# Kernel optimization log

Hardware: AMD Instinct MI355X
Metric: run time of the kernel (lower is better)

The kernel has to match this reference:

```python
import jax, jax.numpy as jnp
import numpy as np


def _dwconv3d(x, w, b):
    # depthwise Conv3d, kernel 3, stride 1, padding 1 (SAME), groups = channels
    groups = x.shape[1]
    y = jax.lax.conv_general_dilated(
        x, w, window_strides=(1, 1, 1), padding='SAME',
        feature_group_count=groups,
        dimension_numbers=('NCDHW', 'OIDHW', 'NCDHW'))
    return y + b[None, :, None, None, None]


def setup_inputs() -> dict:
    key = jax.random.key(0)
    ks = jax.random.split(key, 8)
    B, C, K, D, H, W = 4, 64, 64, 16, 64, 64
    sc = 0.1
    return {
        'x_q': jax.random.normal(ks[0], (B, C, D, H, W), jnp.float32),
        'x_kv': jax.random.normal(ks[1], (B, K, D, H, W), jnp.float32),
        'wq': jax.random.normal(ks[2], (C, 1, 3, 3, 3), jnp.float32) * sc,
        'bq': jax.random.normal(ks[3], (C,), jnp.float32) * sc,
        'wk': jax.random.normal(ks[4], (K, 1, 3, 3, 3), jnp.float32) * sc,
        'bk': jax.random.normal(ks[5], (K,), jnp.float32) * sc,
        'wv': jax.random.normal(ks[6], (K, 1, 3, 3, 3), jnp.float32) * sc,
        'bv': jax.random.normal(ks[7], (K,), jnp.float32) * sc,
    }


def reference(x_q, x_kv, wq, bq, wk, bk, wv, bv):
    q = _dwconv3d(x_q, wq, bq)   # [B,C,D,H,W]
    k = _dwconv3d(x_kv, wk, bk)  # [B,K,D,H,W]
    v = _dwconv3d(x_kv, wv, bv)  # [B,K,D,H,W]
    B, C = q.shape[:2]
    K = k.shape[1]
    qf = q.reshape(B, C, -1)     # [B,C,S]
    kf = k.reshape(B, K, -1)     # [B,K,S]
    vf = v.reshape(B, K, -1)     # [B,K,S]
    attn = jnp.einsum('bcs,bks->bck', qf, kf) / jnp.sqrt(jnp.asarray(K, qf.dtype))
    attn = jax.nn.softmax(attn, axis=-1)           # [B,C,K]
    n = int(0.1 * C)
    at = attn.transpose(0, 2, 1)                   # [B,K,C]
    _, idx = jax.lax.top_k(at, n)                  # [B,K,n] indices into C
    mask = jnp.sum(jax.nn.one_hot(idx, C, dtype=attn.dtype), axis=-2)  # [B,K,C]
    attn_m = attn * mask.transpose(0, 2, 1)        # [B,C,K], NOT renormalized
    out = jnp.einsum('bck,bks->bcs', attn_m, vf).reshape(q.shape)
    return x_q + out, attn_m
```

## Files before the change

### kernel.cpp

```cpp
#include <hip/hip_runtime.h>
#include <math.h>

#define BB   4
#define CC   64
#define KK   64
#define DDim 16
#define HDim 64
#define WDim 64
#define SS   (DDim*HDim*WDim)
#define PLANE (HDim*WDim)
#define NCH2 64
#define TOPN 6
#define RSTR 68
#define RROWS 18
#define NSTG 288

typedef __attribute__((ext_vector_type(8))) short bf16x8;
typedef __attribute__((ext_vector_type(4))) float f32x4;

__device__ __forceinline__ unsigned cvt_pk_bf16(float lo, float hi) {
    unsigned r;
    asm("v_cvt_pk_bf16_f32 %0, %1, %2" : "=v"(r) : "v"(lo), "v"(hi));
    return r;
}
__device__ __forceinline__ float bf2f(unsigned short u) {
    union { unsigned u; float f; } v; v.u = ((unsigned)u) << 16; return v.f;
}

__global__ __launch_bounds__(128) void conv_uni(
    const float* __restrict__ xq, const float* __restrict__ xkv,
    const float* __restrict__ wq, const float* __restrict__ bq,
    const float* __restrict__ wk, const float* __restrict__ bk,
    const float* __restrict__ wv, const float* __restrict__ bv,
    unsigned short* __restrict__ qo, unsigned short* __restrict__ ko,
    unsigned short* __restrict__ vo)
{
    __shared__ float ringQ[4][RROWS*RSTR];
    __shared__ float ringK[4][RROWS*RSTR];

    int bid  = blockIdx.x;
    int work = (bid & 7) * 128 + (bid >> 3);
    int b  = work >> 8;
    int c  = (work >> 2) & 63;
    int hq = work & 3;
    int g0 = hq << 4;

    const float* srcQ = xq  + (size_t)(b*CC + c) * SS;
    const float* srcK = xkv + (size_t)(b*CC + c) * SS;
    float wQ[27], wK[27], wV[27];
    #pragma unroll
    for (int i = 0; i < 27; ++i) {
        wQ[i] = wq[c*27 + i];
        wK[i] = wk[c*27 + i];
        wV[i] = wv[c*27 + i];
    }
    const float bQ = bq[c], bK = bk[c], bV = bv[c];

    unsigned short* dQ = qo + (size_t)(b*CC + c) * SS;
    unsigned short* dK = ko + (size_t)(b*CC + c) * SS;
    unsigned short* dV = vo + (size_t)(b*CC + c) * SS;

    const int tid  = threadIdx.x;
    const int lane = tid & 63;
    const int wg   = tid & 7;
    const int w0   = wg << 3;
    const int hl   = tid >> 3;
    const int y    = g0 + hl;

    float4 stgQ[3], stgK[3];
#define SLOAD2(p) {                                                            \
    const int p_ = (p);                                                        \
    const bool pv_ = (p_ >= 0 && p_ < DDim);                                   \
    _Pragma("unroll")                                                          \
    for (int i_ = 0; i_ < 3; ++i_) {                                           \
        const int fidx_ = i_*128 + tid;                                        \
        const int row_  = fidx_ >> 4;                                          \
        const int gy_   = g0 - 1 + row_;                                       \
        float4 vq_ = make_float4(0.f,0.f,0.f,0.f), vk_ = vq_;                  \
        if (pv_ && fidx_ < NSTG && gy_ >= 0 && gy_ < HDim) {                   \
            const size_t o_ = (size_t)p_*PLANE + gy_*WDim + (fidx_ & 15)*4;    \
            vq_ = *(const float4*)(srcQ + o_);                                 \
            vk_ = *(const float4*)(srcK + o_);                                 \
        }                                                                      \
        stgQ[i_] = vq_; stgK[i_] = vk_;                                        \
    } }
#define SWRITE2(p) {                                                           \
    float* RQ_ = ringQ[(p) & 3];                                               \
    float* RK_ = ringK[(p) & 3];                                               \
    _Pragma("unroll")                                                          \
    for (int i_ = 0; i_ < 3; ++i_) {                                           \
        const int fidx_ = i_*128 + tid;                                        \
        if (fidx_ < NSTG) {                                                    \
            const int off_ = (fidx_ >> 4)*RSTR + (fidx_ & 15)*4;               \
            *(float4*)&RQ_[off_] = stgQ[i_];                                   \
            *(float4*)&RK_[off_] = stgK[i_];                                   \
        }                                                                      \
    } }

#define COMPUTE_D(dd) {                                                        \
    float accQ[8], accK[8], accV[8];                                           \
    _Pragma("unroll")                                                          \
    for (int j = 0; j < 8; ++j) { accQ[j] = bQ; accK[j] = bK; accV[j] = bV; }  \
    _Pragma("unroll")                                                          \
    for (int dz = 0; dz < 3; ++dz) {                                           \
        const float* RQ = ringQ[((dd) + dz + 3) & 3];       \
        const float* RK = ringK[((dd) + dz + 3) & 3];                          \
        _Pragma("unroll")                                                      \
        for (int dy = 0; dy < 3; ++dy) {                                       \
            const int base_ = (hl + dy)*RSTR;                                  \
            float4 qa0 = *(const float4*)&RQ[base_ + w0];                      \
            float4 qa1 = *(const float4*)&RQ[base_ + w0 + 4];                  \
            float4 ka0 = *(const float4*)&RK[base_ + w0];                      \
            float4 ka1 = *(const float4*)&RK[base_ + w0 + 4];                  \
            float qlh = __shfl(qa1.w, lane - 1, 64);                           \
            float qrh = __shfl(qa0.x, lane + 1, 64);                           \
            float klh = __shfl(ka1.w, lane - 1, 64);                           \
            float krh = __shfl(ka0.x, lane + 1, 64);                           \
            float rq[10], rk[10];                                              \
            rq[0] = wg       ? qlh : 0.f;                                      \
            rq[9] = (wg < 7) ? qrh : 0.f;                                      \
            rq[1]=qa0.x; rq[2]=qa0.y; rq[3]=qa0.z; rq[4]=qa0.w;                \
            rq[5]=qa1.x; rq[6]=qa1.y; rq[7]=qa1.z; rq[8]=qa1.w;                \
            rk[0] = wg       ? klh : 0.f;                                      \
            rk[9] = (wg < 7) ? krh : 0.f;                                      \
            rk[1]=ka0.x; rk[2]=ka0.y; rk[3]=ka0.z; rk[4]=ka0.w;                \
            rk[5]=ka1.x; rk[6]=ka1.y; rk[7]=ka1.z; rk[8]=ka1.w;                \
            const float cq0 = wQ[dz*9 + dy*3 + 0];                             \
            const float cq1 = wQ[dz*9 + dy*3 + 1];                             \
            const float cq2 = wQ[dz*9 + dy*3 + 2];                             \
            const float ck0 = wK[dz*9 + dy*3 + 0];                             \
            const float ck1 = wK[dz*9 + dy*3 + 1];                             \
            const float ck2 = wK[dz*9 + dy*3 + 2];                             \
            const float cv0 = wV[dz*9 + dy*3 + 0];                             \
            const float cv1 = wV[dz*9 + dy*3 + 1];                             \
            const float cv2 = wV[dz*9 + dy*3 + 2];                             \
            _Pragma("unroll")                                                  \
            for (int j = 0; j < 8; ++j) {                                      \
                float sQ = fmaf(cq0, rq[j],   accQ[j]);                        \
                sQ       = fmaf(cq1, rq[j+1], sQ);                             \
                accQ[j]  = fmaf(cq2, rq[j+2], sQ);                             \
                float sK = fmaf(ck0, rk[j],   accK[j]);                        \
                sK       = fmaf(ck1, rk[j+1], sK);                             \
                accK[j]  = fmaf(ck2, rk[j+2], sK);                             \
                float sV = fmaf(cv0, rk[j],   accV[j]);                        \
                sV       = fmaf(cv1, rk[j+1], sV);                             \
                accV[j]  = fmaf(cv2, rk[j+2], sV);                             \
            }                                                                  \
        }                                                                      \
    }                                                                          \
    const int off = (dd)*PLANE + y*WDim + w0;                                  \
    uint4 pq, pk, pv;                                                          \
    pq.x = cvt_pk_bf16(accQ[0], accQ[1]);                                      \
    pq.y = cvt_pk_bf16(accQ[2], accQ[3]);                                      \
    pq.z = cvt_pk_bf16(accQ[4], accQ[5]);                                      \
    pq.w = cvt_pk_bf16(accQ[6], accQ[7]);                                      \
    pk.x = cvt_pk_bf16(accK[0], accK[1]);                                      \
    pk.y = cvt_pk_bf16(accK[2], accK[3]);                                      \
    pk.z = cvt_pk_bf16(accK[4], accK[5]);                                      \
    pk.w = cvt_pk_bf16(accK[6], accK[7]);                                      \
    pv.x = cvt_pk_bf16(accV[0], accV[1]);                                      \
    pv.y = cvt_pk_bf16(accV[2], accV[3]);                                      \
    pv.z = cvt_pk_bf16(accV[4], accV[5]);                                      \
    pv.w = cvt_pk_bf16(accV[6], accV[7]);                                      \
    *(uint4*)&dQ[off] = pq;                                                    \
    *(uint4*)&dK[off] = pk;                                                    \
    *(uint4*)&dV[off] = pv;                                                    \
    }

    SLOAD2(-1); SWRITE2(-1);
    SLOAD2(0);  SWRITE2(0);
    SLOAD2(1);  SWRITE2(1);
    __syncthreads();

    for (int d = 0; d < DDim; ++d) {
        if (d < DDim - 1) SLOAD2(d + 2);
        COMPUTE_D(d);
        if (d < DDim - 1) SWRITE2(d + 2);
        __syncthreads();
    }
#undef SLOAD2
#undef SWRITE2
#undef COMPUTE_D
}

__global__ __launch_bounds__(256) void gemm1_mfma(
    const unsigned short* __restrict__ qb, const unsigned short* __restrict__ kb,
    float* __restrict__ part)
{
    __shared__ unsigned short lq[64*136];
    __shared__ unsigned short lk[64*136];

    int bid   = blockIdx.x;
    int b     = bid >> 6;
    int chunk = bid & 63;
    int tid   = threadIdx.x;
    int lane  = tid & 63;
    int wid   = tid >> 6;
    int c0    = wid << 4;
    int lr    = lane & 15;
    int kq    = lane >> 4;

    const unsigned short* qsrc = qb + (size_t)b*CC*SS;
    const unsigned short* ksrc = kb + (size_t)b*KK*SS;

    f32x4 acc[4];
    #pragma unroll
    for (int j = 0; j < 4; ++j) acc[j] = (f32x4){0.f, 0.f, 0.f, 0.f};

    const int sbase = chunk << 10;
    for (int sc = 0; sc < 8; ++sc) {
        const int s0 = sbase + (sc << 7);
        __syncthreads();
        #pragma unroll
        for (int it = 0; it < 8; ++it) {
            const int idx  = it*256 + tid;
            const int tile = idx >> 10;
            const int row  = (idx >> 4) & 63;
            const int ch8  = idx & 15;
            const unsigned short* s_ = (tile ? ksrc : qsrc) + (size_t)row*SS + s0 + ch8*8;
            unsigned short* d_ = (tile ? lk : lq) + row*136 + ch8*8;
            *(uint4*)d_ = *(const uint4*)s_;
        }
        __syncthreads();
        #pragma unroll
        for (int ss = 0; ss < 4; ++ss) {
            const int scol = ss*32 + kq*8;
            bf16x8 a = *(const bf16x8*)&lq[(c0 + lr)*136 + scol];
            #pragma unroll
            for (int j = 0; j < 4; ++j) {
                bf16x8 bv = *(const bf16x8*)&lk[(j*16 + lr)*136 + scol];
                acc[j] = __builtin_amdgcn_mfma_f32_16x16x32_bf16(a, bv, acc[j], 0, 0, 0);
            }
        }
    }

    float* pb = part + ((size_t)(b*NCH2 + chunk)) * (CC*KK);
    #pragma unroll
    for (int j = 0; j < 4; ++j)
        #pragma unroll
        for (int r = 0; r < 4; ++r)
            pb[(c0 + kq*4 + r)*KK + j*16 + lr] = acc[j][r];
}

__global__ __launch_bounds__(256) void reduce_attn(
    const float* __restrict__ part, float* __restrict__ attn)
{
    int bid = blockIdx.x;
    int b = bid >> 6, c = bid & 63;
    int tid = threadIdx.x;
    int k = tid & 63, g = tid >> 6;
    float s = 0.f;
    for (int ch = g; ch < NCH2; ch += 4)
        s += part[(size_t)(b*NCH2 + ch)*(CC*KK) + c*KK + k];
    __shared__ float red[256];
    red[tid] = s;
    __syncthreads();
    if (tid < 64) {
        float tot = red[tid] + red[tid+64] + red[tid+128] + red[tid+192];
        attn[b*CC*KK + c*KK + tid] = tot * 0.125f;
    }
}

__global__ __launch_bounds__(64) void softmax_topk(
    const float* __restrict__ attn, float* __restrict__ attn_m)
{
    __shared__ float p[64*65];
    int b = blockIdx.x;
    int t = threadIdx.x;
    for (int i = 0; i < 64; ++i) p[i*65 + t] = attn[b*4096 + i*64 + t];
    __syncthreads();
    float m = -1e30f;
    for (int k = 0; k < 64; ++k) m = fmaxf(m, p[t*65 + k]);
    float sum = 0.f;
    for (int k = 0; k < 64; ++k) { float e = expf(p[t*65+k] - m); p[t*65+k] = e; sum += e; }
    float inv = 1.f / sum;
    for (int k = 0; k < 64; ++k) p[t*65+k] *= inv;
    __syncthreads();
    unsigned long long chosen = 0ull;
    #pragma unroll
    for (int pass = 0; pass < TOPN; ++pass) {
        float best = -1.f; int bi = 0;
        for (int c2 = 0; c2 < 64; ++c2) {
            float v = p[c2*65 + t];
            if (!((chosen >> c2) & 1ull) && v > best) { best = v; bi = c2; }
        }
        chosen |= 1ull << bi;
    }
    for (int c2 = 0; c2 < 64; ++c2) {
        float v = p[c2*65 + t];
        attn_m[b*4096 + c2*64 + t] = ((chosen >> c2) & 1ull) ? v : 0.f;
    }
}

__global__ __launch_bounds__(256) void gemm2_out(
    const float* __restrict__ attn_m, const unsigned short* __restrict__ v,
    const float* __restrict__ xq, float* __restrict__ out)
{
    __shared__ float amt[64][68];
    __shared__ float vt[64][132];
    int bid = blockIdx.x;
    int b  = bid >> 7;
    int ch = bid & 127;
    int tid = threadIdx.x;
    for (int i = 0; i < 16; ++i) {
        int idx = i*256 + tid;
        amt[idx & 63][idx >> 6] = attn_m[b*4096 + idx];
    }
    int c0 = (tid >> 4) * 4;
    int s0 = (tid & 15) * 8;
    const unsigned short* vb = v + (size_t)b*KK*SS;
    const float* xb = xq + (size_t)b*CC*SS;
    float* ob = out + (size_t)b*CC*SS;
    int sb0 = ch * 512;
    for (int st = 0; st < 4; ++st) {
        int sb = sb0 + st*128;
        __syncthreads();
        #pragma unroll
        for (int i = 0; i < 4; ++i) {
            int idx = i*256 + tid;
            int k   = idx >> 4;
            int s8  = (idx & 15) * 8;
            uint4 pk = *(const uint4*)&vb[(size_t)k*SS + sb + s8];
            float* dst = &vt[k][s8];
            dst[0] = bf2f((unsigned short)(pk.x & 0xffff));
            dst[1] = bf2f((unsigned short)(pk.x >> 16));
            dst[2] = bf2f((unsigned short)(pk.y & 0xffff));
            dst[3] = bf2f((unsigned short)(pk.y >> 16));
            dst[4] = bf2f((unsigned short)(pk.z & 0xffff));
            dst[5] = bf2f((unsigned short)(pk.z >> 16));
            dst[6] = bf2f((unsigned short)(pk.w & 0xffff));
            dst[7] = bf2f((unsigned short)(pk.w >> 16));
        }
        __syncthreads();
        float acc[4][8] = {};
        #pragma unroll 8
        for (int k = 0; k < 64; ++k) {
            float4 a  = *(const float4*)&amt[k][c0];
            float4 v0 = *(const float4*)&vt[k][s0];
            float4 v1 = *(const float4*)&vt[k][s0+4];
            float av[4] = {a.x,a.y,a.z,a.w};
            float vv[8] = {v0.x,v0.y,v0.z,v0.w,v1.x,v1.y,v1.z,v1.w};
            #pragma unroll
            for (int i = 0; i < 4; ++i)
                #pragma unroll
                for (int j = 0; j < 8; ++j)
                    acc[i][j] = fmaf(av[i], vv[j], acc[i][j]);
        }
        #pragma unroll
        for (int i = 0; i < 4; ++i) {
            int off = (c0+i)*SS + sb + s0;
            float4 x0 = *(const float4*)&xb[off];
            float4 x1 = *(const float4*)&xb[off+4];
            *(float4*)&ob[off]   = make_float4(acc[i][0]+x0.x, acc[i][1]+x0.y,
                                               acc[i][2]+x0.z, acc[i][3]+x0.w);
            *(float4*)&ob[off+4] = make_float4(acc[i][4]+x1.x, acc[i][5]+x1.y,
                                               acc[i][6]+x1.z, acc[i][7]+x1.w);
        }
    }
}

extern "C" void kernel_launch(void* const* d_in, const int* in_sizes, int n_in,
                              void* d_out, int out_size, void* d_ws, size_t ws_size,
                              hipStream_t stream)
{
    const float* xq  = (const float*)d_in[0];
    const float* xkv = (const float*)d_in[1];
    const float* wq  = (const float*)d_in[2];
    const float* bq  = (const float*)d_in[3];
    const float* wk  = (const float*)d_in[4];
    const float* bk  = (const float*)d_in[5];
    const float* wv  = (const float*)d_in[6];
    const float* bv  = (const float*)d_in[7];
    float* out = (float*)d_out;

    unsigned short* k_ws = (unsigned short*)d_ws;
    unsigned short* v_ws = k_ws + (size_t)BB*KK*SS;
    float* part = (float*)(v_ws + (size_t)BB*KK*SS);
    float* attn = part + (size_t)BB*NCH2*CC*KK;

    unsigned short* q_bf = (unsigned short*)out;
    float* attn_m = out + (size_t)BB*CC*SS;

    conv_uni   <<<BB*CC*4,   128, 0, stream>>>(xq, xkv, wq, bq, wk, bk, wv, bv,
                                               q_bf, k_ws, v_ws);
    gemm1_mfma <<<BB*NCH2,   256, 0, stream>>>(q_bf, k_ws, part);
    reduce_attn<<<BB*CC,     256, 0, stream>>>(part, attn);
    softmax_topk<<<BB,        64, 0, stream>>>(attn, attn_m);
    gemm2_out  <<<BB*128,    256, 0, stream>>>(attn_m, v_ws, xq, out);
}
```

Measured before the change: 139.9 us.

## Stream conv input planes into LDS via global_load_lds with XOR-swizzled layout

Replaces the register-staged global load plus LDS store in the depthwise conv kernel with direct global-to-LDS DMA loads (global_load_lds, 16 bytes per lane). Out-of-bounds halo rows read from a zeroed scratch page instead of being predicated. Padding is replaced by an XOR swizzle of 16-byte columns so the compute reads stay conflict-free. This removes staging registers and VGPR-to-LDS write instructions, but adds a memset launch and relies on the async DMA completing before the per-plane barrier, which may need explicit vmcnt waits.

```diff
diff --git a/kernel.cpp b/kernel.cpp
--- a/kernel.cpp
+++ b/kernel.cpp
@@ -11,7 +11,6 @@
 #define PLANE (HDim*WDim)
 #define NCH2 64
 #define TOPN 6
-#define RSTR 68
 #define RROWS 18
 #define NSTG 288
 
@@ -26,17 +25,23 @@
 __device__ __forceinline__ float bf2f(unsigned short u) {
     union { unsigned u; float f; } v; v.u = ((unsigned)u) << 16; return v.f;
 }
-
-__global__ __launch_bounds__(128) void conv_uni(
+__device__ __forceinline__ void gld16(const float* g, float* l) {
+    __builtin_amdgcn_global_load_lds(
+        (const __attribute__((address_space(1))) void*)g,
+        (__attribute__((address_space(3))) void*)l, 16, 0, 0);
+}
+
+__global__ __launch_bounds__(128) void conv_dma(
     const float* __restrict__ xq, const float* __restrict__ xkv,
     const float* __restrict__ wq, const float* __restrict__ bq,
     const float* __restrict__ wk, const float* __restrict__ bk,
     const float* __restrict__ wv, const float* __restrict__ bv,
+    const float* __restrict__ zpg,
     unsigned short* __restrict__ qo, unsigned short* __restrict__ ko,
     unsigned short* __restrict__ vo)
 {
-    __shared__ float ringQ[4][RROWS*RSTR];
-    __shared__ float ringK[4][RROWS*RSTR];
+    __shared__ float ringQ[4][RROWS*64];
+    __shared__ float ringK[4][RROWS*64];
 
     int bid  = blockIdx.x;
     int work = (bid & 7) * 128 + (bid >> 3);
@@ -67,33 +72,23 @@
     const int hl   = tid >> 3;
     const int y    = g0 + hl;
 
-    float4 stgQ[3], stgK[3];
-#define SLOAD2(p) {                                                            \
+#define DMA2(p) {                                                              \
     const int p_ = (p);                                                        \
     const bool pv_ = (p_ >= 0 && p_ < DDim);                                   \
-    _Pragma("unroll")                                                          \
-    for (int i_ = 0; i_ < 3; ++i_) {                                           \
-        const int fidx_ = i_*128 + tid;                                        \
-        const int row_  = fidx_ >> 4;                                          \
-        const int gy_   = g0 - 1 + row_;                                       \
-        float4 vq_ = make_float4(0.f,0.f,0.f,0.f), vk_ = vq_;                  \
-        if (pv_ && fidx_ < NSTG && gy_ >= 0 && gy_ < HDim) {                   \
-            const size_t o_ = (size_t)p_*PLANE + gy_*WDim + (fidx_ & 15)*4;    \
-            vq_ = *(const float4*)(srcQ + o_);                                 \
-            vk_ = *(const float4*)(srcK + o_);                                 \
-        }                                                                      \
-        stgQ[i_] = vq_; stgK[i_] = vk_;                                        \
-    } }
-#define SWRITE2(p) {                                                           \
-    float* RQ_ = ringQ[(p) & 3];                                               \
-    float* RK_ = ringK[(p) & 3];                                               \
+    float* LQ_ = ringQ[(p_) & 3];                                              \
+    float* LK_ = ringK[(p_) & 3];                                              \
     _Pragma("unroll")                                                          \
     for (int i_ = 0; i_ < 3; ++i_) {                                           \
         const int fidx_ = i_*128 + tid;                                        \
         if (fidx_ < NSTG) {                                                    \
-            const int off_ = (fidx_ >> 4)*RSTR + (fidx_ & 15)*4;               \
-            *(float4*)&RQ_[off_] = stgQ[i_];                                   \
-            *(float4*)&RK_[off_] = stgK[i_];                                   \
+            const int row_ = fidx_ >> 4;                                       \
+            const int gcc_ = (fidx_ & 15) ^ (row_ & 15);      \
+            const int gy_  = g0 - 1 + row_;                                    \
+            const bool ok_ = pv_ && gy_ >= 0 && gy_ < HDim;                    \
+            const size_t o_ = (size_t)(pv_ ? p_ : 0)*PLANE                     \
+                              + (ok_ ? gy_ : 0)*WDim + gcc_*4;                 \
+            gld16(ok_ ? srcQ + o_ : zpg, LQ_ + fidx_*4);                       \
+            gld16(ok_ ? srcK + o_ : zpg, LK_ + fidx_*4);                       \
         }                                                                      \
     } }
 
@@ -107,11 +102,15 @@
         const float* RK = ringK[((dd) + dz + 3) & 3];                          \
         _Pragma("unroll")                                                      \
         for (int dy = 0; dy < 3; ++dy) {                                       \
-            const int base_ = (hl + dy)*RSTR;                                  \
-            float4 qa0 = *(const float4*)&RQ[base_ + w0];                      \
-            float4 qa1 = *(const float4*)&RQ[base_ + w0 + 4];                  \
-            float4 ka0 = *(const float4*)&RK[base_ + w0];                      \
-            float4 ka1 = *(const float4*)&RK[base_ + w0 + 4];                  \
+            const int row_ = hl + dy;                                          \
+            const int rx_  = row_ & 15;                                        \
+            const int rb_  = row_ << 6;                                        \
+            const int c0_  = ((wg << 1)       ^ rx_) << 2;                     \
+            const int c1_  = (((wg << 1) | 1) ^ rx_) << 2;                     \
+            float4 qa0 = *(const float4*)&RQ[rb_ + c0_];                       \
+            float4 qa1 = *(const float4*)&RQ[rb_ + c1_];                       \
+            float4 ka0 = *(const float4*)&RK[rb_ + c0_];                       \
+            float4 ka1 = *(const float4*)&RK[rb_ + c1_];                       \
             float qlh = __shfl(qa1.w, lane - 1, 64);                           \
             float qrh = __shfl(qa0.x, lane + 1, 64);                           \
             float klh = __shfl(ka1.w, lane - 1, 64);                           \
@@ -167,19 +166,17 @@
     *(uint4*)&dV[off] = pv;                                                    \
     }
 
-    SLOAD2(-1); SWRITE2(-1);
-    SLOAD2(0);  SWRITE2(0);
-    SLOAD2(1);  SWRITE2(1);
+    DMA2(-1);
+    DMA2(0);
+    DMA2(1);
     __syncthreads();
 
     for (int d = 0; d < DDim; ++d) {
-        if (d < DDim - 1) SLOAD2(d + 2);
+        if (d < DDim - 1) DMA2(d + 2);
         COMPUTE_D(d);
-        if (d < DDim - 1) SWRITE2(d + 2);
-        __syncthreads();
-    }
-#undef SLOAD2
-#undef SWRITE2
+        __syncthreads();
+    }
+#undef DMA2
 #undef COMPUTE_D
 }
 
@@ -377,12 +374,15 @@
     unsigned short* v_ws = k_ws + (size_t)BB*KK*SS;
     float* part = (float*)(v_ws + (size_t)BB*KK*SS);
     float* attn = part + (size_t)BB*NCH2*CC*KK;
+    float* zpg  = attn + (size_t)BB*CC*KK;
 
     unsigned short* q_bf = (unsigned short*)out;
     float* attn_m = out + (size_t)BB*CC*SS;
 
-    conv_uni   <<<BB*CC*4,   128, 0, stream>>>(xq, xkv, wq, bq, wk, bk, wv, bv,
-                                               q_bf, k_ws, v_ws);
+    hipMemsetAsync(zpg, 0, 256, stream);
+
+    conv_dma   <<<BB*CC*4,   128, 0, stream>>>(xq, xkv, wq, bq, wk, bk, wv, bv,
+                                               zpg, q_bf, k_ws, v_ws);
     gemm1_mfma <<<BB*NCH2,   256, 0, stream>>>(q_bf, k_ws, part);
     reduce_attn<<<BB*CC,     256, 0, stream>>>(part, attn);
     softmax_topk<<<BB,        64, 0, stream>>>(attn, attn_m);
```

After: 154.9 us. +10.7%, slower.

## Restructure depthwise conv as scatter over input planes with rotating accumulators

Applied to the files above, without the earlier changes.

The conv kernel switches from gathering three input depth planes per output plane to scattering each input plane into three rotating output accumulator sets (previous, current, next). Each LDS plane is read and shuffled once instead of three times, which cuts LDS traffic and shuffle work, and the zero-padding plane loads at the depth boundaries are dropped. The cost is three times the accumulator registers (72 floats), a fully unrolled depth loop and larger code, which may lower occupancy.

```diff
diff --git a/kernel.cpp b/kernel.cpp
--- a/kernel.cpp
+++ b/kernel.cpp
@@ -27,7 +27,7 @@
     union { unsigned u; float f; } v; v.u = ((unsigned)u) << 16; return v.f;
 }
 
-__global__ __launch_bounds__(128) void conv_uni(
+__global__ __launch_bounds__(128) void conv_sct(
     const float* __restrict__ xq, const float* __restrict__ xkv,
     const float* __restrict__ wq, const float* __restrict__ bq,
     const float* __restrict__ wk, const float* __restrict__ bk,
@@ -70,14 +70,13 @@
     float4 stgQ[3], stgK[3];
 #define SLOAD2(p) {                                                            \
     const int p_ = (p);                                                        \
-    const bool pv_ = (p_ >= 0 && p_ < DDim);                                   \
     _Pragma("unroll")                                                          \
     for (int i_ = 0; i_ < 3; ++i_) {                                           \
         const int fidx_ = i_*128 + tid;                                        \
         const int row_  = fidx_ >> 4;                                          \
         const int gy_   = g0 - 1 + row_;                                       \
         float4 vq_ = make_float4(0.f,0.f,0.f,0.f), vk_ = vq_;                  \
-        if (pv_ && fidx_ < NSTG && gy_ >= 0 && gy_ < HDim) {                   \
+        if (fidx_ < NSTG && gy_ >= 0 && gy_ < HDim) {                          \
             const size_t o_ = (size_t)p_*PLANE + gy_*WDim + (fidx_ & 15)*4;    \
             vq_ = *(const float4*)(srcQ + o_);                                 \
             vk_ = *(const float4*)(srcK + o_);                                 \
@@ -97,90 +96,151 @@
         }                                                                      \
     } }
 
-#define COMPUTE_D(dd) {                                                        \
-    float accQ[8], accK[8], accV[8];                                           \
-    _Pragma("unroll")                                                          \
-    for (int j = 0; j < 8; ++j) { accQ[j] = bQ; accK[j] = bK; accV[j] = bV; }  \
-    _Pragma("unroll")                                                          \
-    for (int dz = 0; dz < 3; ++dz) {                                           \
-        const float* RQ = ringQ[((dd) + dz + 3) & 3];       \
-        const float* RK = ringK[((dd) + dz + 3) & 3];                          \
+#define STOREOUT(AQ, AK, AV, dd) {                                             \
+    const int off_ = (dd)*PLANE + y*WDim + w0;                                 \
+    uint4 pq_, pk_, pv_;                                                       \
+    pq_.x = cvt_pk_bf16(AQ[0], AQ[1]);                                         \
+    pq_.y = cvt_pk_bf16(AQ[2], AQ[3]);                                         \
+    pq_.z = cvt_pk_bf16(AQ[4], AQ[5]);                                         \
+    pq_.w = cvt_pk_bf16(AQ[6], AQ[7]);                                         \
+    pk_.x = cvt_pk_bf16(AK[0], AK[1]);                                         \
+    pk_.y = cvt_pk_bf16(AK[2], AK[3]);                                         \
+    pk_.z = cvt_pk_bf16(AK[4], AK[5]);                                         \
+    pk_.w = cvt_pk_bf16(AK[6], AK[7]);                                         \
+    pv_.x = cvt_pk_bf16(AV[0], AV[1]);                                         \
+    pv_.y = cvt_pk_bf16(AV[2], AV[3]);                                         \
+    pv_.z = cvt_pk_bf16(AV[4], AV[5]);                                         \
+    pv_.w = cvt_pk_bf16(AV[6], AV[7]);                                         \
+    *(uint4*)&dQ[off_] = pq_;                                                  \
+    *(uint4*)&dK[off_] = pk_;                                                  \
+    *(uint4*)&dV[off_] = pv_;                                                  \
+    }
+
+#define STEPX(p, PQ,PK,PV, CQ,CK,CV, NQ,NK,NV, DOP, DON) {                     \
+    if (DON) {                                                                 \
         _Pragma("unroll")                                                      \
-        for (int dy = 0; dy < 3; ++dy) {                                       \
-            const int base_ = (hl + dy)*RSTR;                                  \
-            float4 qa0 = *(const float4*)&RQ[base_ + w0];                      \
-            float4 qa1 = *(const float4*)&RQ[base_ + w0 + 4];                  \
-            float4 ka0 = *(const float4*)&RK[base_ + w0];                      \
-            float4 ka1 = *(const float4*)&RK[base_ + w0 + 4];                  \
-            float qlh = __shfl(qa1.w, lane - 1, 64);                           \
-            float qrh = __shfl(qa0.x, lane + 1, 64);                           \
-            float klh = __shfl(ka1.w, lane - 1, 64);                           \
-            float krh = __shfl(ka0.x, lane + 1, 64);                           \
-            float rq[10], rk[10];                                              \
-            rq[0] = wg       ? qlh : 0.f;                                      \
-            rq[9] = (wg < 7) ? qrh : 0.f;                                      \
-            rq[1]=qa0.x; rq[2]=qa0.y; rq[3]=qa0.z; rq[4]=qa0.w;                \
-            rq[5]=qa1.x; rq[6]=qa1.y; rq[7]=qa1.z; rq[8]=qa1.w;                \
-            rk[0] = wg       ? klh : 0.f;                                      \
-            rk[9] = (wg < 7) ? krh : 0.f;                                      \
-            rk[1]=ka0.x; rk[2]=ka0.y; rk[3]=ka0.z; rk[4]=ka0.w;                \
-            rk[5]=ka1.x; rk[6]=ka1.y; rk[7]=ka1.z; rk[8]=ka1.w;                \
-            const float cq0 = wQ[dz*9 + dy*3 + 0];                             \
-            const float cq1 = wQ[dz*9 + dy*3 + 1];                             \
-            const float cq2 = wQ[dz*9 + dy*3 + 2];                             \
-            const float ck0 = wK[dz*9 + dy*3 + 0];                             \
-            const float ck1 = wK[dz*9 + dy*3 + 1];                             \
-            const float ck2 = wK[dz*9 + dy*3 + 2];                             \
-            const float cv0 = wV[dz*9 + dy*3 + 0];                             \
-            const float cv1 = wV[dz*9 + dy*3 + 1];                             \
-            const float cv2 = wV[dz*9 + dy*3 + 2];                             \
+        for (int j = 0; j < 8; ++j) { NQ[j] = bQ; NK[j] = bK; NV[j] = bV; }    \
+    }                                                                          \
+    if ((p) < 14) SLOAD2((p) + 2);               \
+    {         \
+        const float* R_ = ringQ[(p) & 3];                                      \
+        float r_[3][10];                                                       \
+        _Pragma("unroll")                                                      \
+        for (int rr_ = 0; rr_ < 3; ++rr_) {                                    \
+            const int base_ = (hl + rr_)*RSTR + w0;                            \
+            float4 a0_ = *(const float4*)&R_[base_];                           \
+            float4 a1_ = *(const float4*)&R_[base_ + 4];                       \
+            float lh_ = __shfl(a1_.w, lane - 1, 64);                           \
+            float rh_ = __shfl(a0_.x, lane + 1, 64);                           \
+            r_[rr_][0] = wg       ? lh_ : 0.f;                                 \
+            r_[rr_][9] = (wg < 7) ? rh_ : 0.f;                                 \
+            r_[rr_][1]=a0_.x; r_[rr_][2]=a0_.y; r_[rr_][3]=a0_.z;              \
+            r_[rr_][4]=a0_.w; r_[rr_][5]=a1_.x; r_[rr_][6]=a1_.y;              \
+            r_[rr_][7]=a1_.z; r_[rr_][8]=a1_.w;                                \
+        }                                                                      \
+        _Pragma("unroll")                                                      \
+        for (int dy_ = 0; dy_ < 3; ++dy_) {                                    \
             _Pragma("unroll")                                                  \
-            for (int j = 0; j < 8; ++j) {                                      \
-                float sQ = fmaf(cq0, rq[j],   accQ[j]);                        \
-                sQ       = fmaf(cq1, rq[j+1], sQ);                             \
-                accQ[j]  = fmaf(cq2, rq[j+2], sQ);                             \
-                float sK = fmaf(ck0, rk[j],   accK[j]);                        \
-                sK       = fmaf(ck1, rk[j+1], sK);                             \
-                accK[j]  = fmaf(ck2, rk[j+2], sK);                             \
-                float sV = fmaf(cv0, rk[j],   accV[j]);                        \
-                sV       = fmaf(cv1, rk[j+1], sV);                             \
-                accV[j]  = fmaf(cv2, rk[j+2], sV);                             \
+            for (int j_ = 0; j_ < 8; ++j_) {                                   \
+                if (DOP) {                                                     \
+                    float s_ = fmaf(wQ[18+dy_*3+0], r_[dy_][j_],   PQ[j_]);    \
+                    s_       = fmaf(wQ[18+dy_*3+1], r_[dy_][j_+1], s_);        \
+                    PQ[j_]   = fmaf(wQ[18+dy_*3+2], r_[dy_][j_+2], s_);        \
+                }                                                              \
+                {                                                              \
+                    float s_ = fmaf(wQ[9+dy_*3+0], r_[dy_][j_],   CQ[j_]);     \
+                    s_       = fmaf(wQ[9+dy_*3+1], r_[dy_][j_+1], s_);         \
+                    CQ[j_]   = fmaf(wQ[9+dy_*3+2], r_[dy_][j_+2], s_);         \
+                }                                                              \
+                if (DON) {                                                     \
+                    float s_ = fmaf(wQ[0+dy_*3+0], r_[dy_][j_],   NQ[j_]);     \
+                    s_       = fmaf(wQ[0+dy_*3+1], r_[dy_][j_+1], s_);         \
+                    NQ[j_]   = fmaf(wQ[0+dy_*3+2], r_[dy_][j_+2], s_);         \
+                }                                                              \
             }                                                                  \
         }                                                                      \
     }                                                                          \
-    const int off = (dd)*PLANE + y*WDim + w0;                                  \
-    uint4 pq, pk, pv;                                                          \
-    pq.x = cvt_pk_bf16(accQ[0], accQ[1]);                                      \
-    pq.y = cvt_pk_bf16(accQ[2], accQ[3]);                                      \
-    pq.z = cvt_pk_bf16(accQ[4], accQ[5]);                                      \
-    pq.w = cvt_pk_bf16(accQ[6], accQ[7]);                                      \
-    pk.x = cvt_pk_bf16(accK[0], accK[1]);                                      \
-    pk.y = cvt_pk_bf16(accK[2], accK[3]);                                      \
-    pk.z = cvt_pk_bf16(accK[4], accK[5]);                                      \
-    pk.w = cvt_pk_bf16(accK[6], accK[7]);                                      \
-    pv.x = cvt_pk_bf16(accV[0], accV[1]);                                      \
-    pv.y = cvt_pk_bf16(accV[2], accV[3]);                                      \
-    pv.z = cvt_pk_bf16(accV[4], accV[5]);                                      \
-    pv.w = cvt_pk_bf16(accV[6], accV[7]);                                      \
-    *(uint4*)&dQ[off] = pq;                                                    \
-    *(uint4*)&dK[off] = pk;                                                    \
-    *(uint4*)&dV[off] = pv;                                                    \
-    }
-
-    SLOAD2(-1); SWRITE2(-1);
-    SLOAD2(0);  SWRITE2(0);
-    SLOAD2(1);  SWRITE2(1);
+    {                  \
+        const float* R_ = ringK[(p) & 3];                                      \
+        float r_[3][10];                                                       \
+        _Pragma("unroll")                                                      \
+        for (int rr_ = 0; rr_ < 3; ++rr_) {                                    \
+            const int base_ = (hl + rr_)*RSTR + w0;                            \
+            float4 a0_ = *(const float4*)&R_[base_];                           \
+            float4 a1_ = *(const float4*)&R_[base_ + 4];                       \
+            float lh_ = __shfl(a1_.w, lane - 1, 64);                           \
+            float rh_ = __shfl(a0_.x, lane + 1, 64);                           \
+            r_[rr_][0] = wg       ? lh_ : 0.f;                                 \
+            r_[rr_][9] = (wg < 7) ? rh_ : 0.f;                                 \
+            r_[rr_][1]=a0_.x; r_[rr_][2]=a0_.y; r_[rr_][3]=a0_.z;              \
+            r_[rr_][4]=a0_.w; r_[rr_][5]=a1_.x; r_[rr_][6]=a1_.y;              \
+            r_[rr_][7]=a1_.z; r_[rr_][8]=a1_.w;                                \
+        }                                                                      \
+        _Pragma("unroll")                                                      \
+        for (int dy_ = 0; dy_ < 3; ++dy_) {                                    \
+            _Pragma("unroll")                                                  \
+            for (int j_ = 0; j_ < 8; ++j_) {                                   \
+                if (DOP) {                                                     \
+                    float s_ = fmaf(wK[18+dy_*3+0], r_[dy_][j_],   PK[j_]);    \
+                    s_       = fmaf(wK[18+dy_*3+1], r_[dy_][j_+1], s_);        \
+                    PK[j_]   = fmaf(wK[18+dy_*3+2], r_[dy_][j_+2], s_);        \
+                    float t_ = fmaf(wV[18+dy_*3+0], r_[dy_][j_],   PV[j_]);    \
+                    t_       = fmaf(wV[18+dy_*3+1], r_[dy_][j_+1], t_);        \
+                    PV[j_]   = fmaf(wV[18+dy_*3+2], r_[dy_][j_+2], t_);        \
+                }                                                              \
+                {                                                              \
+                    float s_ = fmaf(wK[9+dy_*3+0], r_[dy_][j_],   CK[j_]);     \
+                    s_       = fmaf(wK[9+dy_*3+1], r_[dy_][j_+1], s_);         \
+                    CK[j_]   = fmaf(wK[9+dy_*3+2], r_[dy_][j_+2], s_);         \
+                    float t_ = fmaf(wV[9+dy_*3+0], r_[dy_][j_],   CV[j_]);     \
+                    t_       = fmaf(wV[9+dy_*3+1], r_[dy_][j_+1], t_);         \
+                    CV[j_]   = fmaf(wV[9+dy_*3+2], r_[dy_][j_+2], t_);         \
+                }                                                              \
+                if (DON) {                                                     \
+                    float s_ = fmaf(wK[0+dy_*3+0], r_[dy_][j_],   NK[j_]);     \
+                    s_       = fmaf(wK[0+dy_*3+1], r_[dy_][j_+1], s_);         \
+                    NK[j_]   = fmaf(wK[0+dy_*3+2], r_[dy_][j_+2], s_);         \
+                    float t_ = fmaf(wV[0+dy_*3+0], r_[dy_][j_],   NV[j_]);     \
+                    t_       = fmaf(wV[0+dy_*3+1], r_[dy_][j_+1], t_);         \
+                    NV[j_]   = fmaf(wV[0+dy_*3+2], r_[dy_][j_+2], t_);         \
+                }                                                              \
+            }                                                                  \
+        }                                                                      \
+    }                                                                          \
+    if (DOP) STOREOUT(PQ, PK, PV, (p) - 1);                                    \
+    if ((p) < 14) SWRITE2((p) + 2);                 \
+    if ((p) < 15) __syncthreads();                                             \
+    }
+
+    float aq0[8], ak0[8], av0[8];
+    float aq1[8], ak1[8], av1[8];
+    float aq2[8], ak2[8], av2[8];
+
+    SLOAD2(0); SWRITE2(0);
+    SLOAD2(1); SWRITE2(1);
+    #pragma unroll
+    for (int j = 0; j < 8; ++j) { aq0[j] = bQ; ak0[j] = bK; av0[j] = bV; }
     __syncthreads();
 
-    for (int d = 0; d < DDim; ++d) {
-        if (d < DDim - 1) SLOAD2(d + 2);
-        COMPUTE_D(d);
-        if (d < DDim - 1) SWRITE2(d + 2);
-        __syncthreads();
-    }
+#define S0(p, DOP, DON) STEPX(p, aq2,ak2,av2, aq0,ak0,av0, aq1,ak1,av1, DOP, DON)
+#define S1(p)           STEPX(p, aq0,ak0,av0, aq1,ak1,av1, aq2,ak2,av2, 1, 1)
+#define S2(p)           STEPX(p, aq1,ak1,av1, aq2,ak2,av2, aq0,ak0,av0, 1, 1)
+
+    S0(0, 0, 1); S1(1);  S2(2);
+    S0(3, 1, 1); S1(4);  S2(5);
+    S0(6, 1, 1); S1(7);  S2(8);
+    S0(9, 1, 1); S1(10); S2(11);
+    S0(12, 1, 1); S1(13); S2(14);
+    S0(15, 1, 0);
+    STOREOUT(aq0, ak0, av0, 15);
+
+#undef S0
+#undef S1
+#undef S2
+#undef STEPX
+#undef STOREOUT
 #undef SLOAD2
 #undef SWRITE2
-#undef COMPUTE_D
 }
 
 __global__ __launch_bounds__(256) void gemm1_mfma(
@@ -381,7 +441,7 @@
     unsigned short* q_bf = (unsigned short*)out;
     float* attn_m = out + (size_t)BB*CC*SS;
 
-    conv_uni   <<<BB*CC*4,   128, 0, stream>>>(xq, xkv, wq, bq, wk, bk, wv, bv,
+    conv_sct   <<<BB*CC*4,   128, 0, stream>>>(xq, xkv, wq, bq, wk, bk, wv, bv,
                                                q_bf, k_ws, v_ws);
     gemm1_mfma <<<BB*NCH2,   256, 0, stream>>>(q_bf, k_ws, part);
     reduce_attn<<<BB*CC,     256, 0, stream>>>(part, attn);
```

Result: slower. 224.4 us (+60.4%).

## Load MFMA operands directly from global memory and double split-K chunks in gemm1

Applied to the files above, without the earlier changes.

Removes the LDS staging and the block-wide barriers in the q·kᵀ GEMM. Each wave now reads its bf16 operands straight from global memory into registers for the MFMA. The number of S-chunks per batch doubles to 128, which halves the work per block and raises block count for occupancy. The cost is more partial-sum output for the reduce kernel to sum, plus redundant global K reads across the 4 waves, which the cache must absorb.

```diff
diff --git a/kernel.cpp b/kernel.cpp
--- a/kernel.cpp
+++ b/kernel.cpp
@@ -9,7 +9,7 @@
 #define WDim 64
 #define SS   (DDim*HDim*WDim)
 #define PLANE (HDim*WDim)
-#define NCH2 64
+#define NCH2 128
 #define TOPN 6
 #define RSTR 68
 #define RROWS 18
@@ -187,12 +187,9 @@
     const unsigned short* __restrict__ qb, const unsigned short* __restrict__ kb,
     float* __restrict__ part)
 {
-    __shared__ unsigned short lq[64*136];
-    __shared__ unsigned short lk[64*136];
-
     int bid   = blockIdx.x;
-    int b     = bid >> 6;
-    int chunk = bid & 63;
+    int b     = bid >> 7;
+    int chunk = bid & 127;
     int tid   = threadIdx.x;
     int lane  = tid & 63;
     int wid   = tid >> 6;
@@ -200,37 +197,22 @@
     int lr    = lane & 15;
     int kq    = lane >> 4;
 
-    const unsigned short* qsrc = qb + (size_t)b*CC*SS;
-    const unsigned short* ksrc = kb + (size_t)b*KK*SS;
+    const unsigned short* qrow = qb + (size_t)b*CC*SS + (size_t)(c0 + lr)*SS;
+    const unsigned short* kbb  = kb + (size_t)b*KK*SS;
 
     f32x4 acc[4];
     #pragma unroll
     for (int j = 0; j < 4; ++j) acc[j] = (f32x4){0.f, 0.f, 0.f, 0.f};
 
-    const int sbase = chunk << 10;
-    for (int sc = 0; sc < 8; ++sc) {
-        const int s0 = sbase + (sc << 7);
-        __syncthreads();
+    const int sbase = chunk << 9;
+    #pragma unroll 4
+    for (int t = 0; t < 16; ++t) {
+        const int scol = sbase + t*32 + kq*8;
+        bf16x8 a = *(const bf16x8*)&qrow[scol];
         #pragma unroll
-        for (int it = 0; it < 8; ++it) {
-            const int idx  = it*256 + tid;
-            const int tile = idx >> 10;
-            const int row  = (idx >> 4) & 63;
-            const int ch8  = idx & 15;
-            const unsigned short* s_ = (tile ? ksrc : qsrc) + (size_t)row*SS + s0 + ch8*8;
-            unsigned short* d_ = (tile ? lk : lq) + row*136 + ch8*8;
-            *(uint4*)d_ = *(const uint4*)s_;
-        }
-        __syncthreads();
-        #pragma unroll
-        for (int ss = 0; ss < 4; ++ss) {
-            const int scol = ss*32 + kq*8;
-            bf16x8 a = *(const bf16x8*)&lq[(c0 + lr)*136 + scol];
-            #pragma unroll
-            for (int j = 0; j < 4; ++j) {
-                bf16x8 bv = *(const bf16x8*)&lk[(j*16 + lr)*136 + scol];
-                acc[j] = __builtin_amdgcn_mfma_f32_16x16x32_bf16(a, bv, acc[j], 0, 0, 0);
-            }
+        for (int j = 0; j < 4; ++j) {
+            bf16x8 bv = *(const bf16x8*)&kbb[(size_t)(j*16 + lr)*SS + scol];
+            acc[j] = __builtin_amdgcn_mfma_f32_16x16x32_bf16(a, bv, acc[j], 0, 0, 0);
         }
     }
 
```

Result: slower. 152.9 us (+9.2%).
